# Optimization experiments

Hardware: AMD Instinct MI355X
Metric: run time of the kernel (lower is better)

The kernel has to match this reference:

```python
import jax, jax.numpy as jnp
import numpy as np

N_FEATURE = 12
SIGMA = 0.015
NODES = jnp.linspace(0.0, 0.3, 12)  # RBF centers, matches torch.linspace(0,0.3,12)

B, N, K, FIN = 16, 4096, 32, 4


def setup_inputs() -> dict:
    key = jax.random.key(0)
    ks = jax.random.split(key, 24)

    def make_d(ki, kd):
        idx = jax.random.randint(ki, (B, N, K), 0, N).astype(jnp.float32)
        dist = jax.random.uniform(kd, (B, N, K), minval=0.0, maxval=0.3)
        return jnp.stack([idx, dist], axis=-1)  # [B,N,K,2]

    def lin(kw, kb, fin, fout):
        W = jax.random.normal(kw, (fin, fout), jnp.float32) * (1.0 / np.sqrt(fin))
        b = jax.random.normal(kb, (fout,), jnp.float32) * 0.01
        return W, b

    x = jax.random.normal(ks[0], (B, N, FIN), jnp.float32)
    d1 = make_d(ks[1], ks[2])
    d0 = make_d(ks[3], ks[4])
    dm1 = make_d(ks[5], ks[6])
    mask = jnp.ones((B, N), dtype=bool)

    We, be = lin(ks[7], ks[8], FIN, N_FEATURE)
    Wm1, bm1 = lin(ks[9], ks[10], N_FEATURE + 12, N_FEATURE)
    Wu1, bu1 = lin(ks[11], ks[12], 2 * N_FEATURE, N_FEATURE)
    Wm0, bm0 = lin(ks[13], ks[14], N_FEATURE + 12, N_FEATURE)
    Wu0, bu0 = lin(ks[15], ks[16], 2 * N_FEATURE, N_FEATURE)
    Wmm1, bmm1 = lin(ks[17], ks[18], N_FEATURE + 12, N_FEATURE)
    Wum1, bum1 = lin(ks[19], ks[20], 2 * N_FEATURE, N_FEATURE)

    return {"x": x, "d1": d1, "d0": d0, "dm1": dm1, "mask": mask,
            "We": We, "be": be, "Wm1": Wm1, "bm1": bm1, "Wu1": Wu1, "bu1": bu1,
            "Wm0": Wm0, "bm0": bm0, "Wu0": Wu0, "bu0": bu0,
            "Wmm1": Wmm1, "bmm1": bmm1, "Wum1": Wum1, "bum1": bum1}


def _branch(h, d, Wm, bm, Wu, bu):
    # d: [B,N,K,2] -> channel 0 neighbor index, channel 1 distance
    idx = d[..., 0].astype(jnp.int32)                     # [B,N,K]
    rbf = jnp.exp(-((d[..., 1][..., None] - NODES) ** 2) / (2.0 * SIGMA ** 2))  # [B,N,K,12]
    hj = jax.vmap(lambda hb, ib: hb[ib])(h, idx)          # gather: [B,N,K,F]
    hd = jnp.concatenate([hj, rbf], axis=-1)              # [B,N,K,F+12]
    m = jax.nn.relu(hd @ Wm + bm).sum(axis=2)             # [B,N,F]
    return jax.nn.sigmoid(jnp.concatenate([h, m], axis=-1) @ Wu + bu)  # [B,N,F]


def reference(x, d1, d0, dm1, mask,
              We, be, Wm1, bm1, Wu1, bu1,
              Wm0, bm0, Wu0, bu0,
              Wmm1, bmm1, Wum1, bum1):
    h = jax.nn.relu(x @ We + be)                          # [B,N,12]
    h1 = _branch(h, d1, Wm1, bm1, Wu1, bu1)
    h0 = _branch(h, d0, Wm0, bm0, Wu0, bu0)
    hm1 = _branch(h, dm1, Wmm1, bmm1, Wum1, bum1)
    return (h1, h0, hm1)
```

## Files before the change

### kernel.cpp

```cpp
#include <hip/hip_runtime.h>
#include <hip/hip_fp16.h>
#include <math.h>

#define BBAT 16
#define NNODE 4096
#define KNB 32
#define NF 12
#define TBL 512
#define NPB 820
#define TMAIN 832

#define LDS_BYTES 110616

__device__ __forceinline__ __half2 u2h(unsigned int u) { __half2 h; __builtin_memcpy(&h, &u, 4); return h; }
__device__ __forceinline__ unsigned int h2u(__half2 h) { unsigned int u; __builtin_memcpy(&u, &h, 4); return u; }
__device__ __forceinline__ float4 ldf4(const float* p) { return *(const float4*)p; }

__global__ __launch_bounds__(256) void prep_kernel(
    const float* __restrict__ x, const float* __restrict__ We, const float* __restrict__ be,
    const float* __restrict__ Wm1, const float* __restrict__ bm1,
    const float* __restrict__ Wm0, const float* __restrict__ bm0,
    const float* __restrict__ Wmm1, const float* __restrict__ bmm1,
    float* __restrict__ h, uint4* __restrict__ gA, uint2* __restrict__ gB)
{
    const int node = blockIdx.x * 256 + threadIdx.x;
    float4 xv = ((const float4*)x)[node];
    float hv[NF];
#pragma unroll
    for (int f = 0; f < NF; f++) {
        float s = be[f];
        s = fmaf(xv.x, We[0 * NF + f], s);
        s = fmaf(xv.y, We[1 * NF + f], s);
        s = fmaf(xv.z, We[2 * NF + f], s);
        s = fmaf(xv.w, We[3 * NF + f], s);
        hv[f] = fmaxf(s, 0.0f);
    }
    float4* hp = (float4*)(h + (size_t)node * NF);
    hp[0] = make_float4(hv[0], hv[1], hv[2], hv[3]);
    hp[1] = make_float4(hv[4], hv[5], hv[6], hv[7]);
    hp[2] = make_float4(hv[8], hv[9], hv[10], hv[11]);

#define DO_G(BR, WM, BM) {                                                     \
        float g[NF];                                                           \
        _Pragma("unroll") for (int c = 0; c < NF; c++) {                       \
            float s = BM[c];                                                   \
            _Pragma("unroll") for (int j = 0; j < NF; j++)                     \
                s = fmaf(hv[j], WM[j * NF + c], s);                            \
            g[c] = s;                                                          \
        }                                                                      \
        uint4 a; uint2 bv;                                                     \
        a.x  = h2u(__floats2half2_rn(g[0],  g[1]));                            \
        a.y  = h2u(__floats2half2_rn(g[2],  g[3]));                            \
        a.z  = h2u(__floats2half2_rn(g[4],  g[5]));                            \
        a.w  = h2u(__floats2half2_rn(g[6],  g[7]));                            \
        bv.x = h2u(__floats2half2_rn(g[8],  g[9]));                            \
        bv.y = h2u(__floats2half2_rn(g[10], g[11]));                           \
        gA[(size_t)(BR) * 65536 + node] = a;                                   \
        gB[(size_t)(BR) * 65536 + node] = bv;                                  \
    }
    DO_G(0, Wm1, bm1)
    DO_G(1, Wm0, bm0)
    DO_G(2, Wmm1, bmm1)
#undef DO_G
}

__global__ __launch_bounds__(256) void table_kernel(
    const float* __restrict__ Wm1, const float* __restrict__ Wm0, const float* __restrict__ Wmm1,
    uint4* __restrict__ tA, uint2* __restrict__ tB)
{
    const int br = blockIdx.x;
    const float* Wm = (br == 0) ? Wm1 : (br == 1) ? Wm0 : Wmm1;
    for (int e = threadIdx.x; e < TBL + 1; e += 256) {
        float dd = (float)e * (0.3f / (float)TBL);
        float rbf[12];
#pragma unroll
        for (int j = 0; j < 12; j++) {
            float t = dd - (0.3f / 11.0f) * (float)j;
            rbf[j] = expf(-2222.2222222222f * t * t);
        }
        float ph[NF];
#pragma unroll
        for (int c = 0; c < NF; c++) {
            float s = 0.0f;
#pragma unroll
            for (int j = 0; j < 12; j++) s = fmaf(rbf[j], Wm[(12 + j) * NF + c], s);
            ph[c] = s;
        }
        uint4 a; uint2 bv;
        a.x  = h2u(__floats2half2_rn(ph[0],  ph[1]));
        a.y  = h2u(__floats2half2_rn(ph[2],  ph[3]));
        a.z  = h2u(__floats2half2_rn(ph[4],  ph[5]));
        a.w  = h2u(__floats2half2_rn(ph[6],  ph[7]));
        bv.x = h2u(__floats2half2_rn(ph[8],  ph[9]));
        bv.y = h2u(__floats2half2_rn(ph[10], ph[11]));
        tA[br * (TBL + 1) + e] = a;
        tB[br * (TBL + 1) + e] = bv;
    }
}

__global__ __launch_bounds__(TMAIN) void main_kernel(
    const float* __restrict__ h,
    const uint4* __restrict__ gA, const uint2* __restrict__ gB,
    const uint4* __restrict__ tA, const uint2* __restrict__ tB,
    const float* __restrict__ d1, const float* __restrict__ d0, const float* __restrict__ dm1,
    const float* __restrict__ Wu1, const float* __restrict__ bu1,
    const float* __restrict__ Wu0, const float* __restrict__ bu0,
    const float* __restrict__ Wum1, const float* __restrict__ bum1,
    float* __restrict__ out)
{
    extern __shared__ char smem[];
    uint4* gAl = (uint4*)smem;
    uint2* gBl = (uint2*)(smem + 65536);
    uint4* tAl = (uint4*)(smem + 98304);
    uint2* tBl = (uint2*)(smem + 106512);

    const int q = blockIdx.x, b = blockIdx.y, br = blockIdx.z;
    const int tid = threadIdx.x;
    const size_t slice = (size_t)(br * BBAT + b) * NNODE;

    {
        const uint4* gAg = gA + slice;
        const uint2* gBg = gB + slice;
        for (int i = tid; i < NNODE; i += TMAIN) { gAl[i] = gAg[i]; gBl[i] = gBg[i]; }
        const uint4* tAg = tA + br * (TBL + 1);
        const uint2* tBg = tB + br * (TBL + 1);
        for (int i = tid; i < TBL + 1; i += TMAIN) { tAl[i] = tAg[i]; tBl[i] = tBg[i]; }
    }
    __syncthreads();

    const int n = q * NPB + tid;
    if (tid >= NPB || n >= NNODE) return;

    const float* dsel = (br == 0) ? d1 : (br == 1) ? d0 : dm1;
    const float* Wu   = (br == 0) ? Wu1 : (br == 1) ? Wu0 : Wum1;
    const float* bu   = (br == 0) ? bu1 : (br == 1) ? bu0 : bum1;

    float m[NF];
#pragma unroll
    for (int f = 0; f < NF; f++) m[f] = 0.0f;

    const float4* dp = (const float4*)(dsel + ((size_t)b * NNODE + n) * (size_t)(KNB * 2));

#define ACC(O, G, T0, T1) {                                                    \
        __half2 t0 = u2h(T0), t1 = u2h(T1);                                    \
        __half2 phi = __hfma2(f2, __hsub2(t1, t0), t0);                        \
        __half2 s2 = __hadd2(u2h(G), phi);                                     \
        float2 sf = __half22float2(s2);                                        \
        m[O]     += fmaxf(sf.x, 0.0f);                                         \
        m[O + 1] += fmaxf(sf.y, 0.0f);                                         \
    }

#pragma unroll
    for (int kt = 0; kt < 4; kt++) {
        float4 e0 = dp[kt * 4 + 0];
        float4 e1 = dp[kt * 4 + 1];
        float4 e2 = dp[kt * 4 + 2];
        float4 e3 = dp[kt * 4 + 3];
        float idxf[8] = { e0.x, e0.z, e1.x, e1.z, e2.x, e2.z, e3.x, e3.z };
        float dist[8] = { e0.y, e0.w, e1.y, e1.w, e2.y, e2.w, e3.y, e3.w };
#pragma unroll
        for (int ee = 0; ee < 8; ee++) {
            int j = (int)idxf[ee];
            uint4 ga = gAl[j];
            uint2 gb = gBl[j];
            float uu = dist[ee] * ((float)TBL / 0.3f);
            int i = (int)uu;
            i = min(i, TBL - 1);
            float fr = uu - (float)i;
            __half2 f2 = __float2half2_rn(fr);
            uint4 a0 = tAl[i];
            uint2 b0 = tBl[i];
            uint4 a1 = tAl[i + 1];
            uint2 b1 = tBl[i + 1];
            ACC(0,  ga.x, a0.x, a1.x)
            ACC(2,  ga.y, a0.y, a1.y)
            ACC(4,  ga.z, a0.z, a1.z)
            ACC(6,  ga.w, a0.w, a1.w)
            ACC(8,  gb.x, b0.x, b1.x)
            ACC(10, gb.y, b0.y, b1.y)
        }
    }
#undef ACC

    const float* hp = h + ((size_t)b * NNODE + n) * NF;
    float4 h0 = ldf4(hp), h1v = ldf4(hp + 4), h2v = ldf4(hp + 8);
    float hv[NF] = { h0.x, h0.y, h0.z, h0.w, h1v.x, h1v.y, h1v.z, h1v.w,
                     h2v.x, h2v.y, h2v.z, h2v.w };
    float ov[NF];
#pragma unroll
    for (int f = 0; f < NF; f++) {
        float a = bu[f];
#pragma unroll
        for (int j = 0; j < NF; j++) a = fmaf(hv[j], Wu[j * NF + f], a);
#pragma unroll
        for (int j = 0; j < NF; j++) a = fmaf(m[j], Wu[(NF + j) * NF + f], a);
        ov[f] = 1.0f / (1.0f + __expf(-a));
    }
    float* op = out + (slice + n) * NF;
    ((float4*)op)[0] = make_float4(ov[0], ov[1], ov[2],  ov[3]);
    ((float4*)op)[1] = make_float4(ov[4], ov[5], ov[6],  ov[7]);
    ((float4*)op)[2] = make_float4(ov[8], ov[9], ov[10], ov[11]);
}

extern "C" void kernel_launch(void* const* d_in, const int* in_sizes, int n_in,
                              void* d_out, int out_size, void* d_ws, size_t ws_size,
                              hipStream_t stream)
{
    const float* x    = (const float*)d_in[0];
    const float* d1   = (const float*)d_in[1];
    const float* d0   = (const float*)d_in[2];
    const float* dm1  = (const float*)d_in[3];
    const float* We   = (const float*)d_in[5];
    const float* be   = (const float*)d_in[6];
    const float* Wm1  = (const float*)d_in[7];
    const float* bm1  = (const float*)d_in[8];
    const float* Wu1  = (const float*)d_in[9];
    const float* bu1  = (const float*)d_in[10];
    const float* Wm0  = (const float*)d_in[11];
    const float* bm0  = (const float*)d_in[12];
    const float* Wu0  = (const float*)d_in[13];
    const float* bu0  = (const float*)d_in[14];
    const float* Wmm1 = (const float*)d_in[15];
    const float* bmm1 = (const float*)d_in[16];
    const float* Wum1 = (const float*)d_in[17];
    const float* bum1 = (const float*)d_in[18];

    char* ws = (char*)d_ws;
    float* h  = (float*)ws;
    uint4* gA = (uint4*)(ws + 3145728);
    uint2* gB = (uint2*)(ws + 6291456);
    uint4* tA = (uint4*)(ws + 7864320);
    uint2* tB = (uint2*)(ws + 7888944);

    hipFuncSetAttribute((const void*)main_kernel,
                        hipFuncAttributeMaxDynamicSharedMemorySize, LDS_BYTES);

    prep_kernel<<<dim3(256), 256, 0, stream>>>(
        x, We, be, Wm1, bm1, Wm0, bm0, Wmm1, bmm1, h, gA, gB);
    table_kernel<<<dim3(3), 256, 0, stream>>>(Wm1, Wm0, Wmm1, tA, tB);
    main_kernel<<<dim3(5, BBAT, 3), TMAIN, LDS_BYTES, stream>>>(
        h, gA, gB, tA, tB, d1, d0, dm1,
        Wu1, bu1, Wu0, bu0, Wum1, bum1, (float*)d_out);
}
```

Before: 148.7 us.

## Use nearest-neighbor RBF table lookup and precompute h-part of update per branch

Grows the RBF projection table fourfold and replaces linear interpolation with a nearest-entry lookup, halving table LDS reads and removing the half-precision interpolation math in the inner neighbor loop. The h·Wu+bu half of the update layer is precomputed per branch in the prep kernel and read back in the main kernel, dropping the h buffer. The table kernel is parallelized across more blocks. This trades accuracy (nearest lookup), more LDS per block (possibly lowering occupancy) and extra workspace traffic for less inner-loop work.

```diff
diff --git a/kernel.cpp b/kernel.cpp
--- a/kernel.cpp
+++ b/kernel.cpp
@@ -6,11 +6,11 @@
 #define NNODE 4096
 #define KNB 32
 #define NF 12
-#define TBL 512
+#define TBL 2048
 #define NPB 820
 #define TMAIN 832
 
-#define LDS_BYTES 110616
+#define LDS_BYTES 147480
 
 __device__ __forceinline__ __half2 u2h(unsigned int u) { __half2 h; __builtin_memcpy(&h, &u, 4); return h; }
 __device__ __forceinline__ unsigned int h2u(__half2 h) { unsigned int u; __builtin_memcpy(&u, &h, 4); return u; }
@@ -21,7 +21,10 @@
     const float* __restrict__ Wm1, const float* __restrict__ bm1,
     const float* __restrict__ Wm0, const float* __restrict__ bm0,
     const float* __restrict__ Wmm1, const float* __restrict__ bmm1,
-    float* __restrict__ h, uint4* __restrict__ gA, uint2* __restrict__ gB)
+    const float* __restrict__ Wu1, const float* __restrict__ bu1,
+    const float* __restrict__ Wu0, const float* __restrict__ bu0,
+    const float* __restrict__ Wum1, const float* __restrict__ bum1,
+    uint4* __restrict__ gA, uint2* __restrict__ gB, float* __restrict__ u0)
 {
     const int node = blockIdx.x * 256 + threadIdx.x;
     float4 xv = ((const float4*)x)[node];
@@ -35,18 +38,16 @@
         s = fmaf(xv.w, We[3 * NF + f], s);
         hv[f] = fmaxf(s, 0.0f);
     }
-    float4* hp = (float4*)(h + (size_t)node * NF);
-    hp[0] = make_float4(hv[0], hv[1], hv[2], hv[3]);
-    hp[1] = make_float4(hv[4], hv[5], hv[6], hv[7]);
-    hp[2] = make_float4(hv[8], hv[9], hv[10], hv[11]);
-
-#define DO_G(BR, WM, BM) {                                                     \
-        float g[NF];                                                           \
+
+#define DO_BR(BR, WM, BM, WU, BU) {                                            \
+        float g[NF], u[NF];                                                    \
         _Pragma("unroll") for (int c = 0; c < NF; c++) {                       \
-            float s = BM[c];                                                   \
-            _Pragma("unroll") for (int j = 0; j < NF; j++)                     \
+            float s = BM[c], t = BU[c];                                        \
+            _Pragma("unroll") for (int j = 0; j < NF; j++) {                   \
                 s = fmaf(hv[j], WM[j * NF + c], s);                            \
-            g[c] = s;                                                          \
+                t = fmaf(hv[j], WU[j * NF + c], t);                            \
+            }                                                                  \
+            g[c] = s; u[c] = t;                                                \
         }                                                                      \
         uint4 a; uint2 bv;                                                     \
         a.x  = h2u(__floats2half2_rn(g[0],  g[1]));                            \
@@ -57,11 +58,15 @@
         bv.y = h2u(__floats2half2_rn(g[10], g[11]));                           \
         gA[(size_t)(BR) * 65536 + node] = a;                                   \
         gB[(size_t)(BR) * 65536 + node] = bv;                                  \
-    }
-    DO_G(0, Wm1, bm1)
-    DO_G(1, Wm0, bm0)
-    DO_G(2, Wmm1, bmm1)
-#undef DO_G
+        float4* up = (float4*)(u0 + ((size_t)(BR) * 65536 + node) * NF);       \
+        up[0] = make_float4(u[0], u[1], u[2],  u[3]);                          \
+        up[1] = make_float4(u[4], u[5], u[6],  u[7]);                          \
+        up[2] = make_float4(u[8], u[9], u[10], u[11]);                         \
+    }
+    DO_BR(0, Wm1, bm1, Wu1, bu1)
+    DO_BR(1, Wm0, bm0, Wu0, bu0)
+    DO_BR(2, Wmm1, bmm1, Wum1, bum1)
+#undef DO_BR
 }
 
 __global__ __launch_bounds__(256) void table_kernel(
@@ -69,50 +74,48 @@
     uint4* __restrict__ tA, uint2* __restrict__ tB)
 {
     const int br = blockIdx.x;
+    const int e = blockIdx.y * 256 + threadIdx.x;
+    if (e > TBL) return;
     const float* Wm = (br == 0) ? Wm1 : (br == 1) ? Wm0 : Wmm1;
-    for (int e = threadIdx.x; e < TBL + 1; e += 256) {
-        float dd = (float)e * (0.3f / (float)TBL);
-        float rbf[12];
-#pragma unroll
-        for (int j = 0; j < 12; j++) {
-            float t = dd - (0.3f / 11.0f) * (float)j;
-            rbf[j] = expf(-2222.2222222222f * t * t);
-        }
-        float ph[NF];
-#pragma unroll
-        for (int c = 0; c < NF; c++) {
-            float s = 0.0f;
-#pragma unroll
-            for (int j = 0; j < 12; j++) s = fmaf(rbf[j], Wm[(12 + j) * NF + c], s);
-            ph[c] = s;
-        }
-        uint4 a; uint2 bv;
-        a.x  = h2u(__floats2half2_rn(ph[0],  ph[1]));
-        a.y  = h2u(__floats2half2_rn(ph[2],  ph[3]));
-        a.z  = h2u(__floats2half2_rn(ph[4],  ph[5]));
-        a.w  = h2u(__floats2half2_rn(ph[6],  ph[7]));
-        bv.x = h2u(__floats2half2_rn(ph[8],  ph[9]));
-        bv.y = h2u(__floats2half2_rn(ph[10], ph[11]));
-        tA[br * (TBL + 1) + e] = a;
-        tB[br * (TBL + 1) + e] = bv;
-    }
+    float dd = (float)e * (0.3f / (float)TBL);
+    float rbf[12];
+#pragma unroll
+    for (int j = 0; j < 12; j++) {
+        float t = dd - (0.3f / 11.0f) * (float)j;
+        rbf[j] = expf(-2222.2222222222f * t * t);
+    }
+    float ph[NF];
+#pragma unroll
+    for (int c = 0; c < NF; c++) {
+        float s = 0.0f;
+#pragma unroll
+        for (int j = 0; j < 12; j++) s = fmaf(rbf[j], Wm[(12 + j) * NF + c], s);
+        ph[c] = s;
+    }
+    uint4 a; uint2 bv;
+    a.x  = h2u(__floats2half2_rn(ph[0],  ph[1]));
+    a.y  = h2u(__floats2half2_rn(ph[2],  ph[3]));
+    a.z  = h2u(__floats2half2_rn(ph[4],  ph[5]));
+    a.w  = h2u(__floats2half2_rn(ph[6],  ph[7]));
+    bv.x = h2u(__floats2half2_rn(ph[8],  ph[9]));
+    bv.y = h2u(__floats2half2_rn(ph[10], ph[11]));
+    tA[br * (TBL + 1) + e] = a;
+    tB[br * (TBL + 1) + e] = bv;
 }
 
 __global__ __launch_bounds__(TMAIN) void main_kernel(
-    const float* __restrict__ h,
     const uint4* __restrict__ gA, const uint2* __restrict__ gB,
     const uint4* __restrict__ tA, const uint2* __restrict__ tB,
+    const float* __restrict__ u0,
     const float* __restrict__ d1, const float* __restrict__ d0, const float* __restrict__ dm1,
-    const float* __restrict__ Wu1, const float* __restrict__ bu1,
-    const float* __restrict__ Wu0, const float* __restrict__ bu0,
-    const float* __restrict__ Wum1, const float* __restrict__ bum1,
+    const float* __restrict__ Wu1, const float* __restrict__ Wu0, const float* __restrict__ Wum1,
     float* __restrict__ out)
 {
     extern __shared__ char smem[];
     uint4* gAl = (uint4*)smem;
     uint2* gBl = (uint2*)(smem + 65536);
     uint4* tAl = (uint4*)(smem + 98304);
-    uint2* tBl = (uint2*)(smem + 106512);
+    uint2* tBl = (uint2*)(smem + 131088);
 
     const int q = blockIdx.x, b = blockIdx.y, br = blockIdx.z;
     const int tid = threadIdx.x;
@@ -133,7 +136,6 @@
 
     const float* dsel = (br == 0) ? d1 : (br == 1) ? d0 : dm1;
     const float* Wu   = (br == 0) ? Wu1 : (br == 1) ? Wu0 : Wum1;
-    const float* bu   = (br == 0) ? bu1 : (br == 1) ? bu0 : bum1;
 
     float m[NF];
 #pragma unroll
@@ -141,10 +143,8 @@
 
     const float4* dp = (const float4*)(dsel + ((size_t)b * NNODE + n) * (size_t)(KNB * 2));
 
-#define ACC(O, G, T0, T1) {                                                    \
-        __half2 t0 = u2h(T0), t1 = u2h(T1);                                    \
-        __half2 phi = __hfma2(f2, __hsub2(t1, t0), t0);                        \
-        __half2 s2 = __hadd2(u2h(G), phi);                                     \
+#define ACC2(O, G, T) {                                                        \
+        __half2 s2 = __hadd2(u2h(G), u2h(T));                                  \
         float2 sf = __half22float2(s2);                                        \
         m[O]     += fmaxf(sf.x, 0.0f);                                         \
         m[O + 1] += fmaxf(sf.y, 0.0f);                                         \
@@ -161,37 +161,31 @@
 #pragma unroll
         for (int ee = 0; ee < 8; ee++) {
             int j = (int)idxf[ee];
+            float uu = dist[ee] * ((float)TBL / 0.3f);
+            int i = (int)(uu + 0.5f);
+            i = min(i, TBL);
             uint4 ga = gAl[j];
             uint2 gb = gBl[j];
-            float uu = dist[ee] * ((float)TBL / 0.3f);
-            int i = (int)uu;
-            i = min(i, TBL - 1);
-            float fr = uu - (float)i;
-            __half2 f2 = __float2half2_rn(fr);
-            uint4 a0 = tAl[i];
-            uint2 b0 = tBl[i];
-            uint4 a1 = tAl[i + 1];
-            uint2 b1 = tBl[i + 1];
-            ACC(0,  ga.x, a0.x, a1.x)
-            ACC(2,  ga.y, a0.y, a1.y)
-            ACC(4,  ga.z, a0.z, a1.z)
-            ACC(6,  ga.w, a0.w, a1.w)
-            ACC(8,  gb.x, b0.x, b1.x)
-            ACC(10, gb.y, b0.y, b1.y)
+            uint4 ta = tAl[i];
+            uint2 tb = tBl[i];
+            ACC2(0,  ga.x, ta.x)
+            ACC2(2,  ga.y, ta.y)
+            ACC2(4,  ga.z, ta.z)
+            ACC2(6,  ga.w, ta.w)
+            ACC2(8,  gb.x, tb.x)
+            ACC2(10, gb.y, tb.y)
         }
     }
-#undef ACC
-
-    const float* hp = h + ((size_t)b * NNODE + n) * NF;
-    float4 h0 = ldf4(hp), h1v = ldf4(hp + 4), h2v = ldf4(hp + 8);
-    float hv[NF] = { h0.x, h0.y, h0.z, h0.w, h1v.x, h1v.y, h1v.z, h1v.w,
-                     h2v.x, h2v.y, h2v.z, h2v.w };
+#undef ACC2
+
+    const float* up = u0 + (slice + n) * NF;
+    float4 ua = ldf4(up), ub = ldf4(up + 4), uc = ldf4(up + 8);
+    float uv[NF] = { ua.x, ua.y, ua.z, ua.w, ub.x, ub.y, ub.z, ub.w,
+                     uc.x, uc.y, uc.z, uc.w };
     float ov[NF];
 #pragma unroll
     for (int f = 0; f < NF; f++) {
-        float a = bu[f];
-#pragma unroll
-        for (int j = 0; j < NF; j++) a = fmaf(hv[j], Wu[j * NF + f], a);
+        float a = uv[f];
 #pragma unroll
         for (int j = 0; j < NF; j++) a = fmaf(m[j], Wu[(NF + j) * NF + f], a);
         ov[f] = 1.0f / (1.0f + __expf(-a));
@@ -226,19 +220,19 @@
     const float* bum1 = (const float*)d_in[18];
 
     char* ws = (char*)d_ws;
-    float* h  = (float*)ws;
-    uint4* gA = (uint4*)(ws + 3145728);
-    uint2* gB = (uint2*)(ws + 6291456);
-    uint4* tA = (uint4*)(ws + 7864320);
-    uint2* tB = (uint2*)(ws + 7888944);
+    uint4* gA = (uint4*)ws;
+    uint2* gB = (uint2*)(ws + 3145728);
+    float* u0 = (float*)(ws + 4718592);
+    uint4* tA = (uint4*)(ws + 14155776);
+    uint2* tB = (uint2*)(ws + 14254128);
 
     hipFuncSetAttribute((const void*)main_kernel,
                         hipFuncAttributeMaxDynamicSharedMemorySize, LDS_BYTES);
 
     prep_kernel<<<dim3(256), 256, 0, stream>>>(
-        x, We, be, Wm1, bm1, Wm0, bm0, Wmm1, bmm1, h, gA, gB);
-    table_kernel<<<dim3(3), 256, 0, stream>>>(Wm1, Wm0, Wmm1, tA, tB);
+        x, We, be, Wm1, bm1, Wm0, bm0, Wmm1, bmm1,
+        Wu1, bu1, Wu0, bu0, Wum1, bum1, gA, gB, u0);
+    table_kernel<<<dim3(3, 9), 256, 0, stream>>>(Wm1, Wm0, Wmm1, tA, tB);
     main_kernel<<<dim3(5, BBAT, 3), TMAIN, LDS_BYTES, stream>>>(
-        h, gA, gB, tA, tB, d1, d0, dm1,
-        Wu1, bu1, Wu0, bu0, Wum1, bum1, (float*)d_out);
-}
+        gA, gB, tA, tB, u0, d1, d0, dm1, Wu1, Wu0, Wum1, (float*)d_out);
+}
```

New measurement: 151.2 us. No clear change (+1.7%).
